# Kernel optimization log

Measured on AMD Instinct MI355X. Metric: run time of the kernel, lower is better.

Reference implementation:

```python
import jax, jax.numpy as jnp
import numpy as np

EPS = 1e-5

def channel_norm(x):
    # per-(batch,channel) norm over spatial dims; torch.var default is unbiased (ddof=1)
    mn = x.mean(axis=(-1, -2), keepdims=True)
    std = jnp.sqrt(x.var(axis=(-1, -2), keepdims=True, ddof=1) + EPS)
    return (x - mn) / std

def conv1x1(x, W, b):
    # x: [B,C,H,W], W: [O,C], b: [O]
    return jnp.einsum('oc,bchw->bohw', W, x) + b[None, :, None, None]

def setup_inputs() -> dict:
    key = jax.random.key(0)
    ks = jax.random.split(key, 10)
    B, C, H, W = 4, 512, 64, 64
    s = 1.0 / np.sqrt(C)  # kaiming-uniform-ish scale for 1x1 conv
    inp = {
        'f_c': jax.random.normal(ks[0], (B, C, H, W), jnp.float32),
        'f_s': jax.random.normal(ks[1], (B, C, H, W), jnp.float32),
        'W_c1': jax.random.uniform(ks[2], (C, C), jnp.float32, -s, s),
        'b_c1': jax.random.uniform(ks[3], (C,), jnp.float32, -s, s),
        'W_s1': jax.random.uniform(ks[4], (C, C), jnp.float32, -s, s),
        'b_s1': jax.random.uniform(ks[5], (C,), jnp.float32, -s, s),
        'W_s2': jax.random.uniform(ks[6], (C, C), jnp.float32, -s, s),
        'b_s2': jax.random.uniform(ks[7], (C,), jnp.float32, -s, s),
        'W_csc': jax.random.uniform(ks[8], (C, C), jnp.float32, -s, s),
        'b_csc': jax.random.uniform(ks[9], (C,), jnp.float32, -s, s),
    }
    return inp

def reference(f_c, f_s, W_c1, b_c1, W_s1, b_s1, W_s2, b_s2, W_csc, b_csc):
    B, C, H, W = f_c.shape
    f_c_hat = channel_norm(f_c)
    f_s_hat = channel_norm(f_s)
    f = conv1x1(f_c_hat, W_c1, b_c1).reshape(B, C, H * W)  # queries [B,C,N]
    g = conv1x1(f_s_hat, W_s1, b_s1).reshape(B, C, H * W)  # keys    [B,C,N]
    scores = jnp.einsum('bci,bcj->bij', f, g)              # [B,N,N]
    attention = jax.nn.softmax(scores, axis=-1)
    h = conv1x1(f_s_hat, W_s2, b_s2).reshape(B, C, H * W)  # values  [B,C,N]
    out = jnp.einsum('bcj,bij->bci', h, attention).reshape(B, C, H, W)
    return conv1x1(out, W_csc, b_csc) + f_c
```

## Files before the change

kernel.cpp:

```cpp
#include <hip/hip_runtime.h>

typedef unsigned short u16;
typedef __attribute__((ext_vector_type(8))) _Float16 f16x8;
typedef __attribute__((ext_vector_type(16))) float f32x16;

#define N_SP 4096
#define C_CH 512
#define B_SZ 4

struct PtrTab { u16* p[4]; };

__device__ __forceinline__ u16 f2h(float f) {
    union { _Float16 h; u16 u; } x; x.h = (_Float16)f; return x.u;
}
__device__ __forceinline__ float h2f(u16 u) {
    union { u16 u; _Float16 h; } x; x.u = u; return (float)x.h;
}
__device__ __forceinline__ void async_cp16(const void* g, void* l) {
    __builtin_amdgcn_global_load_lds((const __attribute__((address_space(1))) unsigned*)g,
                                     (__attribute__((address_space(3))) unsigned*)l, 16, 0, 0);
}
__device__ __forceinline__ float wave_reduce_sum(float v) {
    #pragma unroll
    for (int off = 32; off; off >>= 1) v += __shfl_xor(v, off, 64);
    return v;
}
__device__ __forceinline__ float wave_reduce_max(float v) {
    #pragma unroll
    for (int off = 32; off; off >>= 1) v = fmaxf(v, __shfl_xor(v, off, 64));
    return v;
}

__global__ __launch_bounds__(256) void transpose_cast_stats(
        const float* __restrict__ fc, const float* __restrict__ fs,
        u16* __restrict__ xc, u16* __restrict__ xs,
        float* __restrict__ part_s, float* __restrict__ part_ss) {
    __shared__ float tile[64][65];
    const int t = threadIdx.x;
    const int n0 = blockIdx.x * 64, c0 = blockIdx.y * 64;
    const int z = blockIdx.z;
    const int b = z & 3, which = z >> 2;
    const float* src = which ? fs : fc;
    u16* dst = which ? xs : xc;
    const int r = t >> 4, q4 = (t & 15) * 4;
    #pragma unroll
    for (int it = 0; it < 4; ++it) {
        const int row = it * 16 + r;
        float4 v = *(const float4*)(src + ((size_t)b * C_CH + c0 + row) * N_SP + n0 + q4);
        tile[row][q4 + 0] = v.x; tile[row][q4 + 1] = v.y;
        tile[row][q4 + 2] = v.z; tile[row][q4 + 3] = v.w;
    }
    __syncthreads();
    {
        const int cr = t >> 2, q = t & 3;
        float s = 0.f, ss = 0.f;
        #pragma unroll
        for (int i = 0; i < 16; ++i) {
            float a = tile[cr][q * 16 + i];
            s += a; ss += a * a;
        }
        s += __shfl_xor(s, 1, 64);  s += __shfl_xor(s, 2, 64);
        ss += __shfl_xor(ss, 1, 64); ss += __shfl_xor(ss, 2, 64);
        if (q == 0) {
            atomicAdd(&part_s[z * 512 + c0 + cr], s);
            atomicAdd(&part_ss[z * 512 + c0 + cr], ss);
        }
    }
    #pragma unroll
    for (int it = 0; it < 4; ++it) {
        const int nrow = it * 16 + r;
        ushort4 h4;
        h4.x = f2h(tile[q4 + 0][nrow]);
        h4.y = f2h(tile[q4 + 1][nrow]);
        h4.z = f2h(tile[q4 + 2][nrow]);
        h4.w = f2h(tile[q4 + 3][nrow]);
        *(ushort4*)(dst + ((size_t)b * N_SP + n0 + nrow) * C_CH + c0 + q4) = h4;
    }
}

__global__ __launch_bounds__(256) void prep1(
        const float* __restrict__ W_c1, const float* __restrict__ W_s1,
        const float* __restrict__ W_s2, const float* __restrict__ W_csc,
        const float* __restrict__ b_c1, const float* __restrict__ b_s2,
        const float* __restrict__ b_csc,
        u16* __restrict__ Wbase,
        const float* __restrict__ part_s, const float* __restrict__ part_ss,
        float* __restrict__ mu_a, float* __restrict__ rs_a,
        float* __restrict__ w_u, float* __restrict__ bfold0) {
    __shared__ float tile[64][65];
    const int t = threadIdx.x, z = blockIdx.z;
    if (z < 4) {
        const int n0 = blockIdx.x * 64, c0 = blockIdx.y * 64;
        const float* W = (z == 0) ? W_c1 : (z == 1) ? W_s1 : (z == 2) ? W_s2 : W_csc;
        u16* D = Wbase + ((z == 0) ? 2 : (z == 1) ? 0 : (z == 2) ? 3 : 1) * 262144;
        const int r = t >> 4, q4 = (t & 15) * 4;
        #pragma unroll
        for (int it = 0; it < 4; ++it) {
            const int row = it * 16 + r;
            float4 v = *(const float4*)(W + (size_t)(c0 + row) * 512 + n0 + q4);
            if (z == 3) {
                ushort4 h4 = { f2h(v.x), f2h(v.y), f2h(v.z), f2h(v.w) };
                *(ushort4*)(D + (size_t)(c0 + row) * 512 + n0 + q4) = h4;
            } else {
                tile[row][q4 + 0] = v.x; tile[row][q4 + 1] = v.y;
                tile[row][q4 + 2] = v.z; tile[row][q4 + 3] = v.w;
            }
        }
        __syncthreads();
        if (z == 3) return;
        #pragma unroll
        for (int it = 0; it < 4; ++it) {
            const int nrow = it * 16 + r;
            ushort4 h4;
            h4.x = f2h(tile[q4 + 0][nrow]);
            h4.y = f2h(tile[q4 + 1][nrow]);
            h4.z = f2h(tile[q4 + 2][nrow]);
            h4.w = f2h(tile[q4 + 3][nrow]);
            *(ushort4*)(D + (size_t)(n0 + nrow) * 512 + c0 + q4) = h4;
        }
        return;
    }
    const int flat = blockIdx.y * 8 + blockIdx.x;
    if (flat < 8) {
        #pragma unroll
        for (int h = 0; h < 2; ++h) {
            const int c = flat * 512 + h * 256 + t;
            const float S = part_s[c], SS = part_ss[c];
            const float mean = S * (1.f / N_SP);
            const float var = (SS - S * mean) * (1.f / (N_SP - 1));
            mu_a[c] = mean;
            rs_a[c] = rsqrtf(var + 1e-5f);
        }
    } else if (flat < 10) {
        const int d = (flat - 8) * 256 + t;
        float acc = 0.f;
        for (int o = 0; o < 512; ++o) acc += b_c1[o] * W_s1[(size_t)o * 512 + d];
        w_u[d] = acc;
    } else if (flat < 42) {
        const int w4 = t >> 6, l = t & 63;
        #pragma unroll
        for (int q = 0; q < 4; ++q) {
            const int o = (flat - 10) * 16 + w4 * 4 + q;
            const float4 w0 = *(const float4*)(W_csc + (size_t)o * 512 + l * 8);
            const float4 w1 = *(const float4*)(W_csc + (size_t)o * 512 + l * 8 + 4);
            const float4 b0 = *(const float4*)(b_s2 + l * 8);
            const float4 b1 = *(const float4*)(b_s2 + l * 8 + 4);
            float acc = w0.x * b0.x + w0.y * b0.y + w0.z * b0.z + w0.w * b0.w
                      + w1.x * b1.x + w1.y * b1.y + w1.z * b1.z + w1.w * b1.w;
            acc = wave_reduce_sum(acc);
            if (l == 0) bfold0[o] = acc + b_csc[o];
        }
    }
}

__global__ __launch_bounds__(256) void prep2(
        const u16* __restrict__ WqT16, const u16* __restrict__ Wf16,
        const u16* __restrict__ xs,
        const float* __restrict__ mu_a, const float* __restrict__ rs_a,
        const float* __restrict__ bfold0, const float* __restrict__ w_u,
        u16* __restrict__ Wq_z, u16* __restrict__ Wf_z,
        float* __restrict__ bq, float* __restrict__ bh, float* __restrict__ u_) {
    const int id = blockIdx.x, t = threadIdx.x;
    if (id < 1024) {
        const int y = id >> 9;
        const size_t e = ((size_t)(id & 511) * 256 + t) * 8;
        const int z = (int)(e >> 18), rem = (int)(e & 262143);
        const int d = rem >> 9, a0 = rem & 511;
        u16 v[8];
        if (y == 0) {
            *(uint4*)v = *(const uint4*)(WqT16 + rem);
            const float rd = rs_a[(4 + z) * 512 + d];
            const float* rc = rs_a + z * 512 + a0;
            #pragma unroll
            for (int i = 0; i < 8; ++i) v[i] = f2h(h2f(v[i]) * rc[i] * rd);
            *(uint4*)(Wq_z + e) = *(const uint4*)v;
        } else {
            *(uint4*)v = *(const uint4*)(Wf16 + rem);
            const float* rk = rs_a + (4 + z) * 512 + a0;
            #pragma unroll
            for (int i = 0; i < 8; ++i) v[i] = f2h(h2f(v[i]) * rk[i]);
            *(uint4*)(Wf_z + e) = *(const uint4*)v;
        }
    } else if (id < 2048) {
        const int w = t >> 6, l = t & 63;
        const int oid = (id - 1024) * 4 + w;
        const int kind = oid >> 11;
        const int z = (oid >> 9) & 3, d = oid & 511;
        const u16* row = (kind == 0 ? WqT16 : Wf16) + (size_t)d * 512;
        const int sb = (kind == 0 ? z : 4 + z) * 512;
        float acc = 0.f;
        #pragma unroll
        for (int i = 0; i < 8; ++i) {
            const int a = l * 8 + i;
            acc += h2f(row[a]) * mu_a[sb + a] * rs_a[sb + a];
        }
        acc = wave_reduce_sum(acc);
        if (l == 0) {
            if (kind == 0) bq[z * 512 + d] = -acc * rs_a[(4 + z) * 512 + d];
            else           bh[z * 512 + d] = bfold0[d] - acc;
        }
    } else {
        const int id2 = id - 2048;
        const int b = id2 >> 6, xblk = id2 & 63;
        const int w = t >> 6, l = t & 63;
        float4 u0 = *(const float4*)(w_u + l * 8);
        float4 u1 = *(const float4*)(w_u + l * 8 + 4);
        const float4 r0 = *(const float4*)(rs_a + (4 + b) * 512 + l * 8);
        const float4 r1 = *(const float4*)(rs_a + (4 + b) * 512 + l * 8 + 4);
        u0.x *= r0.x; u0.y *= r0.y; u0.z *= r0.z; u0.w *= r0.w;
        u1.x *= r1.x; u1.y *= r1.y; u1.z *= r1.z; u1.w *= r1.w;
        #pragma unroll
        for (int jj = 0; jj < 16; ++jj) {
            const int j = xblk * 64 + w * 16 + jj;
            const u16* row = xs + ((size_t)b * N_SP + j) * C_CH + l * 8;
            f16x8 x = *(const f16x8*)row;
            float acc = (float)x[0] * u0.x + (float)x[1] * u0.y + (float)x[2] * u0.z + (float)x[3] * u0.w
                      + (float)x[4] * u1.x + (float)x[5] * u1.y + (float)x[6] * u1.z + (float)x[7] * u1.w;
            acc = wave_reduce_sum(acc);
            if (l == 0) u_[(size_t)b * N_SP + j] = acc;
        }
    }
}

enum { OUT_F32 = 0, OUT_F16 = 1 };

template<int OUTMODE, bool TABB, bool TABD>
__global__ __launch_bounds__(256) void gemm_bt(
    const u16* __restrict__ A, const u16* __restrict__ B, PtrTab tab,
    float* __restrict__ Df, u16* __restrict__ Dh,
    const float* __restrict__ bias_m, const float* __restrict__ bias_n,
    const float* __restrict__ res,
    int M, int N, int K, int lda, int ldb, int ldd,
    size_t sA, size_t sB, size_t sD, size_t sR, int sBm, int sBn)
{
    constexpr int TM = 128, TN = 128, BK = 64;
    __shared__ u16 smem[(TM + TN) * BK];
    u16* As = smem;
    u16* Bs = smem + TM * BK;

    const int t = threadIdx.x;
    const int l = t & 63, w = t >> 6;
    const int m0 = blockIdx.y * TM, n0 = blockIdx.x * TN;
    const size_t zb = blockIdx.z;
    const u16* pA = A + zb * sA + (size_t)m0 * lda;
    const u16* pB = (TABB ? tab.p[zb] : B + zb * sB) + (size_t)n0 * ldb;

    const int wr = (w & 1) * 64, wc = (w >> 1) * 64;

    f32x16 acc[2][2] = {};

    for (int k0 = 0; k0 < K; k0 += BK) {
        #pragma unroll
        for (int it = 0; it < 4; ++it) {
            const int L = it * 256 + t;
            const int row = L >> 3, c = L & 7;
            const int sc = (c ^ (row & 7)) * 8;
            async_cp16(pA + (size_t)row * lda + k0 + sc, As + L * 8);
        }
        #pragma unroll
        for (int it = 0; it < 4; ++it) {
            const int L = it * 256 + t;
            const int row = L >> 3, c = L & 7;
            const int sc = (c ^ (row & 7)) * 8;
            async_cp16(pB + (size_t)row * ldb + k0 + sc, Bs + L * 8);
        }
        __syncthreads();
        #pragma unroll
        for (int kk = 0; kk < 4; ++kk) {
            f16x8 af[2], bf[2];
            #pragma unroll
            for (int i = 0; i < 2; ++i) {
                const int row = wr + i * 32 + (l & 31);
                const int ch = ((kk * 2 + (l >> 5)) ^ (row & 7)) * 8;
                af[i] = *(const f16x8*)(As + row * BK + ch);
            }
            #pragma unroll
            for (int j = 0; j < 2; ++j) {
                const int row = wc + j * 32 + (l & 31);
                const int ch = ((kk * 2 + (l >> 5)) ^ (row & 7)) * 8;
                bf[j] = *(const f16x8*)(Bs + row * BK + ch);
            }
            #pragma unroll
            for (int i = 0; i < 2; ++i)
                #pragma unroll
                for (int j = 0; j < 2; ++j)
                    acc[i][j] = __builtin_amdgcn_mfma_f32_32x32x16_f16(af[i], bf[j], acc[i][j], 0, 0, 0);
        }
        __syncthreads();
    }

    const int cl = l & 31, rh = (l >> 5) * 4;
    u16* pDh = (OUTMODE == OUT_F16) ? (TABD ? tab.p[zb] : Dh + zb * sD) : nullptr;
    float* pDf = (OUTMODE == OUT_F32) ? (Df + zb * sD) : nullptr;
    #pragma unroll
    for (int i = 0; i < 2; ++i) {
        #pragma unroll
        for (int j = 0; j < 2; ++j) {
            const int nn = n0 + wc + j * 32 + cl;
            const float bn = bias_n ? bias_n[(size_t)sBn * zb + nn] : 0.f;
            #pragma unroll
            for (int reg = 0; reg < 16; ++reg) {
                const int ml = (reg & 3) + 8 * (reg >> 2) + rh;
                const int mm = m0 + wr + i * 32 + ml;
                float v = acc[i][j][reg] + bn;
                if (bias_m) v += bias_m[(size_t)sBm * zb + mm];
                const size_t off = (size_t)mm * ldd + nn;
                if (OUTMODE == OUT_F32) {
                    if (res) v += res[zb * sR + off];
                    pDf[off] = v;
                } else {
                    pDh[off] = f2h(v);
                }
            }
        }
    }
}

__global__ __launch_bounds__(256) void softmax_kernel(PtrTab tab) {
    u16* row = tab.p[blockIdx.y] + (size_t)blockIdx.x * N_SP;
    const int t = threadIdx.x;
    u16 raw[16];
    *(uint4*)(raw + 0) = *(const uint4*)(row + t * 16);
    *(uint4*)(raw + 8) = *(const uint4*)(row + t * 16 + 8);
    float v[16];
    float mx = -1e30f;
    #pragma unroll
    for (int i = 0; i < 16; ++i) { v[i] = h2f(raw[i]); mx = fmaxf(mx, v[i]); }
    mx = wave_reduce_max(mx);
    __shared__ float red[4];
    const int wave = t >> 6;
    if ((t & 63) == 0) red[wave] = mx;
    __syncthreads();
    mx = fmaxf(fmaxf(red[0], red[1]), fmaxf(red[2], red[3]));
    float sum = 0.f;
    #pragma unroll
    for (int i = 0; i < 16; ++i) { v[i] = __expf(v[i] - mx); sum += v[i]; }
    sum = wave_reduce_sum(sum);
    __syncthreads();
    if ((t & 63) == 0) red[wave] = sum;
    __syncthreads();
    const float inv = 1.f / (red[0] + red[1] + red[2] + red[3]);
    #pragma unroll
    for (int i = 0; i < 16; ++i) raw[i] = f2h(v[i] * inv);
    *(uint4*)(row + t * 16)     = *(const uint4*)(raw + 0);
    *(uint4*)(row + t * 16 + 8) = *(const uint4*)(raw + 8);
}

extern "C" void kernel_launch(void* const* d_in, const int* in_sizes, int n_in,
                              void* d_out, int out_size, void* d_ws, size_t ws_size,
                              hipStream_t stream) {
    const float* f_c   = (const float*)d_in[0];
    const float* f_s   = (const float*)d_in[1];
    const float* W_c1  = (const float*)d_in[2];
    const float* b_c1  = (const float*)d_in[3];
    const float* W_s1  = (const float*)d_in[4];
    const float* b_s1  = (const float*)d_in[5]; (void)b_s1;
    const float* W_s2  = (const float*)d_in[6];
    const float* b_s2  = (const float*)d_in[7];
    const float* W_csc = (const float*)d_in[8];
    const float* b_csc = (const float*)d_in[9];

    const size_t PB = (size_t)N_SP * C_CH;
    const size_t M1 = 1024 * 1024;

    u16* ws   = (u16*)d_ws;
    u16* Xs   = ws;
    u16* q_   = ws + 8 * M1;
    u16* hc   = ws + 16 * M1;
    u16* Xc   = ws + 24 * M1;
    u16* S3   = ws + 24 * M1;
    u16* S0   = ws + 40 * M1;
    u16* S1   = ws + 56 * M1;
    u16* S2   = ws + 72 * M1;
    u16* Wbase= ws + 88 * M1;
    u16* WqT16= Wbase + 4 * 262144;
    u16* Wf16 = Wbase + 5 * 262144;
    u16* Wq_z = Wbase + 6 * 262144;
    u16* Wf_z = Wq_z + 1048576;
    float* f32b = (float*)(ws + 92 * M1);
    float* part_s  = f32b;
    float* part_ss = f32b + 4096;
    float* mu_a    = f32b + 8192;
    float* rs_a    = f32b + 12288;
    float* w_u     = f32b + 16384;
    float* bfold0  = f32b + 16896;
    float* bq      = f32b + 17408;
    float* bh      = f32b + 19456;
    float* u_      = f32b + 21504;

    PtrTab Stab; Stab.p[0] = S0; Stab.p[1] = S1; Stab.p[2] = S2; Stab.p[3] = S3;
    PtrTab tab0 = Stab;

    hipMemsetAsync(part_s, 0, 2 * 4096 * sizeof(float), stream);

    transpose_cast_stats<<<dim3(64, 8, 8), 256, 0, stream>>>(f_c, f_s, Xc, Xs, part_s, part_ss);

    prep1<<<dim3(8, 8, 5), 256, 0, stream>>>(W_c1, W_s1, W_s2, W_csc, b_c1, b_s2, b_csc,
                                             Wbase, part_s, part_ss, mu_a, rs_a, w_u, bfold0);

    gemm_bt<OUT_F16, false, false><<<dim3(4, 4, 2), 256, 0, stream>>>(
        Wbase, Wbase + 2 * 262144, tab0, nullptr, WqT16, nullptr, nullptr, nullptr,
        512, 512, 512, 512, 512, 512, 262144, 262144, 262144, 0, 0, 0);

    prep2<<<2304, 256, 0, stream>>>(WqT16, Wf16, Xs, mu_a, rs_a, bfold0, w_u,
                                    Wq_z, Wf_z, bq, bh, u_);

    gemm_bt<OUT_F16, false, false><<<dim3(4, 32, B_SZ), 256, 0, stream>>>(
        Xc, Wq_z, tab0, nullptr, q_, nullptr, bq, nullptr,
        N_SP, C_CH, C_CH, C_CH, C_CH, C_CH, PB, 262144, PB, 0, 0, 512);
    gemm_bt<OUT_F16, false, false><<<dim3(32, 4, B_SZ), 256, 0, stream>>>(
        Wf_z, Xs, tab0, nullptr, hc, bh, nullptr, nullptr,
        C_CH, N_SP, C_CH, C_CH, C_CH, N_SP, 262144, PB, PB, 0, 512, 0);

    gemm_bt<OUT_F16, false, true><<<dim3(32, 32, B_SZ), 256, 0, stream>>>(
        q_, Xs, Stab, nullptr, nullptr, nullptr, u_, nullptr,
        N_SP, N_SP, C_CH, C_CH, C_CH, N_SP, PB, PB, 0, 0, 0, N_SP);

    softmax_kernel<<<dim3(N_SP, B_SZ), 256, 0, stream>>>(Stab);

    gemm_bt<OUT_F32, true, false><<<dim3(32, 4, B_SZ), 256, 0, stream>>>(
        hc, nullptr, Stab, (float*)d_out, nullptr, nullptr, nullptr, f_c,
        C_CH, N_SP, N_SP, N_SP, N_SP, N_SP, PB, 0, PB, PB, 0, 0);
}
```

Measured before the change: 450.8 us.

## Fuse softmax into score GEMM epilogue with per-tile max/sum correction

The separate softmax pass over the full N×N score matrix is removed. The scores GEMM epilogue now computes per-128-column-tile row maxima, writes exp(s - tile_max) in fp16, and stores partial max and sum values. A small reduce kernel turns these into per-tile correction factors, which the PV GEMM applies while loading the probability tiles into LDS. This saves a full read and write of the scores, but the PV B-operand load becomes synchronous with conversion instead of async global-to-LDS, and the epilogue adds shuffle and LDS reductions.

```diff
diff --git a/kernel.cpp b/kernel.cpp
--- a/kernel.cpp
+++ b/kernel.cpp
@@ -23,11 +23,6 @@
 __device__ __forceinline__ float wave_reduce_sum(float v) {
     #pragma unroll
     for (int off = 32; off; off >>= 1) v += __shfl_xor(v, off, 64);
-    return v;
-}
-__device__ __forceinline__ float wave_reduce_max(float v) {
-    #pragma unroll
-    for (int off = 32; off; off >>= 1) v = fmaxf(v, __shfl_xor(v, off, 64));
     return v;
 }
 
@@ -222,16 +217,11 @@
     }
 }
 
-enum { OUT_F32 = 0, OUT_F16 = 1 };
-
-template<int OUTMODE, bool TABB, bool TABD>
-__global__ __launch_bounds__(256) void gemm_bt(
-    const u16* __restrict__ A, const u16* __restrict__ B, PtrTab tab,
-    float* __restrict__ Df, u16* __restrict__ Dh,
+__global__ __launch_bounds__(256) void gemm_conv(
+    const u16* __restrict__ A, const u16* __restrict__ B, u16* __restrict__ Dh,
     const float* __restrict__ bias_m, const float* __restrict__ bias_n,
-    const float* __restrict__ res,
-    int M, int N, int K, int lda, int ldb, int ldd,
-    size_t sA, size_t sB, size_t sD, size_t sR, int sBm, int sBn)
+    int lda, int ldb, int ldd,
+    size_t sA, size_t sB, size_t sD, int sBm, int sBn, int K)
 {
     constexpr int TM = 128, TN = 128, BK = 64;
     __shared__ u16 smem[(TM + TN) * BK];
@@ -243,8 +233,7 @@
     const int m0 = blockIdx.y * TM, n0 = blockIdx.x * TN;
     const size_t zb = blockIdx.z;
     const u16* pA = A + zb * sA + (size_t)m0 * lda;
-    const u16* pB = (TABB ? tab.p[zb] : B + zb * sB) + (size_t)n0 * ldb;
-
+    const u16* pB = B + zb * sB + (size_t)n0 * ldb;
     const int wr = (w & 1) * 64, wc = (w >> 1) * 64;
 
     f32x16 acc[2][2] = {};
@@ -290,8 +279,7 @@
     }
 
     const int cl = l & 31, rh = (l >> 5) * 4;
-    u16* pDh = (OUTMODE == OUT_F16) ? (TABD ? tab.p[zb] : Dh + zb * sD) : nullptr;
-    float* pDf = (OUTMODE == OUT_F32) ? (Df + zb * sD) : nullptr;
+    u16* pDh = Dh + zb * sD;
     #pragma unroll
     for (int i = 0; i < 2; ++i) {
         #pragma unroll
@@ -304,46 +292,252 @@
                 const int mm = m0 + wr + i * 32 + ml;
                 float v = acc[i][j][reg] + bn;
                 if (bias_m) v += bias_m[(size_t)sBm * zb + mm];
-                const size_t off = (size_t)mm * ldd + nn;
-                if (OUTMODE == OUT_F32) {
-                    if (res) v += res[zb * sR + off];
-                    pDf[off] = v;
-                } else {
-                    pDh[off] = f2h(v);
+                pDh[(size_t)mm * ldd + nn] = f2h(v);
+            }
+        }
+    }
+}
+
+__global__ __launch_bounds__(256) void gemm_scores(
+    const u16* __restrict__ A, const u16* __restrict__ B, PtrTab Stab,
+    const float* __restrict__ u_,
+    float* __restrict__ part_m, float* __restrict__ part_l)
+{
+    constexpr int TM = 128, TN = 128, BK = 64, K = C_CH;
+    __shared__ u16 smem[(TM + TN) * BK];
+    u16* As = smem;
+    u16* Bs = smem + TM * BK;
+
+    const int t = threadIdx.x;
+    const int l = t & 63, w = t >> 6;
+    const int m0 = blockIdx.y * TM, n0 = blockIdx.x * TN;
+    const size_t zb = blockIdx.z;
+    const u16* pA = A + zb * (size_t)(N_SP * C_CH) + (size_t)m0 * C_CH;
+    const u16* pB = B + zb * (size_t)(N_SP * C_CH) + (size_t)n0 * C_CH;
+    const int wr = (w & 1) * 64, wc = (w >> 1) * 64;
+
+    f32x16 acc[2][2] = {};
+
+    for (int k0 = 0; k0 < K; k0 += BK) {
+        #pragma unroll
+        for (int it = 0; it < 4; ++it) {
+            const int L = it * 256 + t;
+            const int row = L >> 3, c = L & 7;
+            const int sc = (c ^ (row & 7)) * 8;
+            async_cp16(pA + (size_t)row * C_CH + k0 + sc, As + L * 8);
+        }
+        #pragma unroll
+        for (int it = 0; it < 4; ++it) {
+            const int L = it * 256 + t;
+            const int row = L >> 3, c = L & 7;
+            const int sc = (c ^ (row & 7)) * 8;
+            async_cp16(pB + (size_t)row * C_CH + k0 + sc, Bs + L * 8);
+        }
+        __syncthreads();
+        #pragma unroll
+        for (int kk = 0; kk < 4; ++kk) {
+            f16x8 af[2], bf[2];
+            #pragma unroll
+            for (int i = 0; i < 2; ++i) {
+                const int row = wr + i * 32 + (l & 31);
+                const int ch = ((kk * 2 + (l >> 5)) ^ (row & 7)) * 8;
+                af[i] = *(const f16x8*)(As + row * BK + ch);
+            }
+            #pragma unroll
+            for (int j = 0; j < 2; ++j) {
+                const int row = wc + j * 32 + (l & 31);
+                const int ch = ((kk * 2 + (l >> 5)) ^ (row & 7)) * 8;
+                bf[j] = *(const f16x8*)(Bs + row * BK + ch);
+            }
+            #pragma unroll
+            for (int i = 0; i < 2; ++i)
+                #pragma unroll
+                for (int j = 0; j < 2; ++j)
+                    acc[i][j] = __builtin_amdgcn_mfma_f32_32x32x16_f16(af[i], bf[j], acc[i][j], 0, 0, 0);
+        }
+        __syncthreads();
+    }
+
+    const int cl = l & 31, h = l >> 5;
+    const float uj0 = u_[zb * N_SP + n0 + wc + cl];
+    const float uj1 = u_[zb * N_SP + n0 + wc + 32 + cl];
+    float* red_m = (float*)smem;
+    float* red_l = red_m + 128;
+
+    float lm[2][16];
+    #pragma unroll
+    for (int i = 0; i < 2; ++i)
+        #pragma unroll
+        for (int r = 0; r < 16; ++r) {
+            float a0 = acc[i][0][r] + uj0;
+            float a1 = acc[i][1][r] + uj1;
+            acc[i][0][r] = a0; acc[i][1][r] = a1;
+            float m = fmaxf(a0, a1);
+            #pragma unroll
+            for (int off = 1; off <= 16; off <<= 1) m = fmaxf(m, __shfl_xor(m, off, 64));
+            lm[i][r] = m;
+        }
+    if (w < 2) {
+        #pragma unroll
+        for (int i = 0; i < 2; ++i)
+            #pragma unroll
+            for (int r = 0; r < 16; ++r)
+                if (cl == 0) red_m[wr + i * 32 + (r & 3) + 8 * (r >> 2) + 4 * h] = lm[i][r];
+    }
+    __syncthreads();
+    if (w >= 2) {
+        #pragma unroll
+        for (int i = 0; i < 2; ++i)
+            #pragma unroll
+            for (int r = 0; r < 16; ++r)
+                if (cl == 0) {
+                    const int rr = wr + i * 32 + (r & 3) + 8 * (r >> 2) + 4 * h;
+                    red_m[rr] = fmaxf(red_m[rr], lm[i][r]);
                 }
-            }
-        }
-    }
-}
-
-__global__ __launch_bounds__(256) void softmax_kernel(PtrTab tab) {
-    u16* row = tab.p[blockIdx.y] + (size_t)blockIdx.x * N_SP;
+    }
+    __syncthreads();
+    u16* pP = Stab.p[zb];
+    float ls[2][16];
+    #pragma unroll
+    for (int i = 0; i < 2; ++i)
+        #pragma unroll
+        for (int r = 0; r < 16; ++r) {
+            const int rr = wr + i * 32 + (r & 3) + 8 * (r >> 2) + 4 * h;
+            const float m = red_m[rr];
+            const float e0 = __expf(acc[i][0][r] - m);
+            const float e1 = __expf(acc[i][1][r] - m);
+            const size_t rowbase = (size_t)(m0 + rr) * N_SP + n0 + wc;
+            pP[rowbase + cl] = f2h(e0);
+            pP[rowbase + 32 + cl] = f2h(e1);
+            float s = e0 + e1;
+            #pragma unroll
+            for (int off = 1; off <= 16; off <<= 1) s += __shfl_xor(s, off, 64);
+            ls[i][r] = s;
+        }
+    if (w < 2) {
+        #pragma unroll
+        for (int i = 0; i < 2; ++i)
+            #pragma unroll
+            for (int r = 0; r < 16; ++r)
+                if (cl == 0) red_l[wr + i * 32 + (r & 3) + 8 * (r >> 2) + 4 * h] = ls[i][r];
+    }
+    __syncthreads();
+    if (w >= 2) {
+        #pragma unroll
+        for (int i = 0; i < 2; ++i)
+            #pragma unroll
+            for (int r = 0; r < 16; ++r)
+                if (cl == 0) {
+                    const int rr = wr + i * 32 + (r & 3) + 8 * (r >> 2) + 4 * h;
+                    const size_t base = ((size_t)zb * N_SP + m0 + rr) * 32 + blockIdx.x;
+                    part_m[base] = red_m[rr];
+                    part_l[base] = red_l[rr] + ls[i][r];
+                }
+    }
+}
+
+__global__ __launch_bounds__(256) void reduce_corr(const float* __restrict__ part_m,
+                                                   const float* __restrict__ part_l,
+                                                   float* __restrict__ corr) {
     const int t = threadIdx.x;
-    u16 raw[16];
-    *(uint4*)(raw + 0) = *(const uint4*)(row + t * 16);
-    *(uint4*)(raw + 8) = *(const uint4*)(row + t * 16 + 8);
-    float v[16];
-    float mx = -1e30f;
-    #pragma unroll
-    for (int i = 0; i < 16; ++i) { v[i] = h2f(raw[i]); mx = fmaxf(mx, v[i]); }
-    mx = wave_reduce_max(mx);
-    __shared__ float red[4];
-    const int wave = t >> 6;
-    if ((t & 63) == 0) red[wave] = mx;
-    __syncthreads();
-    mx = fmaxf(fmaxf(red[0], red[1]), fmaxf(red[2], red[3]));
-    float sum = 0.f;
-    #pragma unroll
-    for (int i = 0; i < 16; ++i) { v[i] = __expf(v[i] - mx); sum += v[i]; }
-    sum = wave_reduce_sum(sum);
-    __syncthreads();
-    if ((t & 63) == 0) red[wave] = sum;
-    __syncthreads();
-    const float inv = 1.f / (red[0] + red[1] + red[2] + red[3]);
-    #pragma unroll
-    for (int i = 0; i < 16; ++i) raw[i] = f2h(v[i] * inv);
-    *(uint4*)(row + t * 16)     = *(const uint4*)(raw + 0);
-    *(uint4*)(row + t * 16 + 8) = *(const uint4*)(raw + 8);
+    const int half = t >> 5, cl = t & 31;
+    const size_t row = (size_t)blockIdx.x * 8 + half;
+    const float m = part_m[row * 32 + cl];
+    const float lsum = part_l[row * 32 + cl];
+    float mm = m;
+    #pragma unroll
+    for (int off = 1; off <= 16; off <<= 1) mm = fmaxf(mm, __shfl_xor(mm, off, 64));
+    const float e = __expf(m - mm);
+    float tot = lsum * e;
+    #pragma unroll
+    for (int off = 1; off <= 16; off <<= 1) tot += __shfl_xor(tot, off, 64);
+    corr[row * 32 + cl] = e / tot;
+}
+
+__global__ __launch_bounds__(256) void gemm_pv(
+    const u16* __restrict__ A , PtrTab Stab, const float* __restrict__ corr,
+    float* __restrict__ out, const float* __restrict__ res)
+{
+    constexpr int TM = 128, TN = 128, BK = 64, K = N_SP;
+    __shared__ u16 smem[(TM + TN) * BK];
+    u16* As = smem;
+    u16* Bs = smem + TM * BK;
+
+    const int t = threadIdx.x;
+    const int l = t & 63, w = t >> 6;
+    const int m0 = blockIdx.y * TM, n0 = blockIdx.x * TN;
+    const size_t zb = blockIdx.z;
+    const size_t PB = (size_t)N_SP * C_CH;
+    const u16* pA = A + zb * PB + (size_t)m0 * N_SP;
+    const u16* pB = Stab.p[zb] + (size_t)n0 * N_SP;
+    const float* pc = corr + ((size_t)zb * N_SP + n0) * 32;
+    const int wr = (w & 1) * 64, wc = (w >> 1) * 64;
+
+    f32x16 acc[2][2] = {};
+
+    for (int k0 = 0; k0 < K; k0 += BK) {
+        #pragma unroll
+        for (int it = 0; it < 4; ++it) {
+            const int L = it * 256 + t;
+            const int row = L >> 3, c = L & 7;
+            const int sc = (c ^ (row & 7)) * 8;
+            async_cp16(pA + (size_t)row * N_SP + k0 + sc, As + L * 8);
+        }
+        const int jblk = k0 >> 7;
+        #pragma unroll
+        for (int it = 0; it < 4; ++it) {
+            const int L = it * 256 + t;
+            const int row = L >> 3, c = L & 7;
+            const int sc = (c ^ (row & 7)) * 8;
+            const float cr = pc[row * 32 + jblk];
+            f16x8 x = *(const f16x8*)(pB + (size_t)row * N_SP + k0 + sc);
+            f16x8 y;
+            #pragma unroll
+            for (int e = 0; e < 8; ++e) y[e] = (_Float16)((float)x[e] * cr);
+            *(f16x8*)(Bs + (size_t)L * 8) = y;
+        }
+        __syncthreads();
+        #pragma unroll
+        for (int kk = 0; kk < 4; ++kk) {
+            f16x8 af[2], bf[2];
+            #pragma unroll
+            for (int i = 0; i < 2; ++i) {
+                const int row = wr + i * 32 + (l & 31);
+                const int ch = ((kk * 2 + (l >> 5)) ^ (row & 7)) * 8;
+                af[i] = *(const f16x8*)(As + row * BK + ch);
+            }
+            #pragma unroll
+            for (int j = 0; j < 2; ++j) {
+                const int row = wc + j * 32 + (l & 31);
+                const int ch = ((kk * 2 + (l >> 5)) ^ (row & 7)) * 8;
+                bf[j] = *(const f16x8*)(Bs + row * BK + ch);
+            }
+            #pragma unroll
+            for (int i = 0; i < 2; ++i)
+                #pragma unroll
+                for (int j = 0; j < 2; ++j)
+                    acc[i][j] = __builtin_amdgcn_mfma_f32_32x32x16_f16(af[i], bf[j], acc[i][j], 0, 0, 0);
+        }
+        __syncthreads();
+    }
+
+    const int cl = l & 31, rh = (l >> 5) * 4;
+    float* pDf = out + zb * PB;
+    const float* pR = res + zb * PB;
+    #pragma unroll
+    for (int i = 0; i < 2; ++i) {
+        #pragma unroll
+        for (int j = 0; j < 2; ++j) {
+            const int nn = n0 + wc + j * 32 + cl;
+            #pragma unroll
+            for (int reg = 0; reg < 16; ++reg) {
+                const int ml = (reg & 3) + 8 * (reg >> 2) + rh;
+                const int mm = m0 + wr + i * 32 + ml;
+                const size_t off = (size_t)mm * N_SP + nn;
+                pDf[off] = acc[i][j][reg] + pR[off];
+            }
+        }
+    }
 }
 
 extern "C" void kernel_launch(void* const* d_in, const int* in_sizes, int n_in,
@@ -387,9 +581,11 @@
     float* bq      = f32b + 17408;
     float* bh      = f32b + 19456;
     float* u_      = f32b + 21504;
+    float* part_m  = f32b + 65536;
+    float* part_l  = part_m + 524288;
+    float* corr    = part_l + 524288;
 
     PtrTab Stab; Stab.p[0] = S0; Stab.p[1] = S1; Stab.p[2] = S2; Stab.p[3] = S3;
-    PtrTab tab0 = Stab;
 
     hipMemsetAsync(part_s, 0, 2 * 4096 * sizeof(float), stream);
 
@@ -398,27 +594,23 @@
     prep1<<<dim3(8, 8, 5), 256, 0, stream>>>(W_c1, W_s1, W_s2, W_csc, b_c1, b_s2, b_csc,
                                              Wbase, part_s, part_ss, mu_a, rs_a, w_u, bfold0);
 
-    gemm_bt<OUT_F16, false, false><<<dim3(4, 4, 2), 256, 0, stream>>>(
-        Wbase, Wbase + 2 * 262144, tab0, nullptr, WqT16, nullptr, nullptr, nullptr,
-        512, 512, 512, 512, 512, 512, 262144, 262144, 262144, 0, 0, 0);
+    gemm_conv<<<dim3(4, 4, 2), 256, 0, stream>>>(
+        Wbase, Wbase + 2 * 262144, WqT16, nullptr, nullptr,
+        512, 512, 512, 262144, 262144, 262144, 0, 0, 512);
 
     prep2<<<2304, 256, 0, stream>>>(WqT16, Wf16, Xs, mu_a, rs_a, bfold0, w_u,
                                     Wq_z, Wf_z, bq, bh, u_);
 
-    gemm_bt<OUT_F16, false, false><<<dim3(4, 32, B_SZ), 256, 0, stream>>>(
-        Xc, Wq_z, tab0, nullptr, q_, nullptr, bq, nullptr,
-        N_SP, C_CH, C_CH, C_CH, C_CH, C_CH, PB, 262144, PB, 0, 0, 512);
-    gemm_bt<OUT_F16, false, false><<<dim3(32, 4, B_SZ), 256, 0, stream>>>(
-        Wf_z, Xs, tab0, nullptr, hc, bh, nullptr, nullptr,
-        C_CH, N_SP, C_CH, C_CH, C_CH, N_SP, 262144, PB, PB, 0, 512, 0);
-
-    gemm_bt<OUT_F16, false, true><<<dim3(32, 32, B_SZ), 256, 0, stream>>>(
-        q_, Xs, Stab, nullptr, nullptr, nullptr, u_, nullptr,
-        N_SP, N_SP, C_CH, C_CH, C_CH, N_SP, PB, PB, 0, 0, 0, N_SP);
-
-    softmax_kernel<<<dim3(N_SP, B_SZ), 256, 0, stream>>>(Stab);
-
-    gemm_bt<OUT_F32, true, false><<<dim3(32, 4, B_SZ), 256, 0, stream>>>(
-        hc, nullptr, Stab, (float*)d_out, nullptr, nullptr, nullptr, f_c,
-        C_CH, N_SP, N_SP, N_SP, N_SP, N_SP, PB, 0, PB, PB, 0, 0);
-}
+    gemm_conv<<<dim3(4, 32, B_SZ), 256, 0, stream>>>(
+        Xc, Wq_z, q_, nullptr, bq,
+        C_CH, C_CH, C_CH, PB, 262144, PB, 0, 512, 512);
+    gemm_conv<<<dim3(32, 4, B_SZ), 256, 0, stream>>>(
+        Wf_z, Xs, hc, bh, nullptr,
+        C_CH, C_CH, N_SP, 262144, PB, PB, 512, 0, 512);
+
+    gemm_scores<<<dim3(32, 32, B_SZ), 256, 0, stream>>>(q_, Xs, Stab, u_, part_m, part_l);
+
+    reduce_corr<<<2048, 256, 0, stream>>>(part_m, part_l, corr);
+
+    gemm_pv<<<dim3(32, 4, B_SZ), 256, 0, stream>>>(hc, Stab, corr, (float*)d_out, f_c);
+}
```

Result: slower. 476.1 us (+5.6%).
